# Optimization experiments

Measured on AMD Instinct MI355X. Metric: run time of the kernel, lower is better.

Reference implementation:

```python
import jax, jax.numpy as jnp
import numpy as np
import math

B, S, D, H, NL, DFF, C, K = 32, 1024, 512, 8, 6, 2048, 128, 8
HD = D // H  # head_dim = 64
EPS = 1e-5


def setup_inputs() -> dict:
    key = jax.random.key(0)
    ks = jax.random.split(key, 24)
    n = lambda k, shape, s=0.02: jax.random.normal(k, shape, jnp.float32) * s
    return {
        'theta': jax.random.uniform(ks[0], (B, S), jnp.float32, -math.pi, math.pi),
        'cond': jax.random.normal(ks[1], (B, C), jnp.float32),
        'attn_bias': jax.random.normal(ks[2], (H, S, S), jnp.float32) * 0.1,
        'embed_W': n(ks[3], (2, D)), 'embed_b': jnp.zeros((D,), jnp.float32),
        'ln1_g': jnp.ones((NL, D), jnp.float32), 'ln1_b': jnp.zeros((NL, D), jnp.float32),
        'ada1_W': n(ks[4], (NL, C, 2 * D)), 'ada1_b': jnp.zeros((NL, 2 * D), jnp.float32),
        'Wq': n(ks[5], (NL, D, D)), 'bq': jnp.zeros((NL, D), jnp.float32),
        'Wk': n(ks[6], (NL, D, D)), 'bk': jnp.zeros((NL, D), jnp.float32),
        'Wv': n(ks[7], (NL, D, D)), 'bv': jnp.zeros((NL, D), jnp.float32),
        'Wo': n(ks[8], (NL, D, D)), 'bo': jnp.zeros((NL, D), jnp.float32),
        'ln2_g': jnp.ones((NL, D), jnp.float32), 'ln2_b': jnp.zeros((NL, D), jnp.float32),
        'ada2_W': n(ks[9], (NL, C, 2 * D)), 'ada2_b': jnp.zeros((NL, 2 * D), jnp.float32),
        'W1': n(ks[10], (NL, D, DFF)), 'b1': jnp.zeros((NL, DFF), jnp.float32),
        'W2': n(ks[11], (NL, DFF, D)), 'b2': jnp.zeros((NL, D), jnp.float32),
        'fn_g': jnp.ones((D,), jnp.float32), 'fn_b': jnp.zeros((D,), jnp.float32),
        'head_W': n(ks[12], (D, 3 * K)), 'head_b': jnp.zeros((3 * K,), jnp.float32),
    }


def _layer_norm(x, g, b):
    m = jnp.mean(x, axis=-1, keepdims=True)
    v = jnp.mean(jnp.square(x - m), axis=-1, keepdims=True)
    return (x - m) * jax.lax.rsqrt(v + EPS) * g + b


def _adaln(x, cond, g, b, pW, pb):
    # AdaLN(x, c) = (1 + scale(c)) * LN(x) + shift(c)
    ss = cond @ pW + pb                      # [B, 2D]
    scale, shift = jnp.split(ss, 2, axis=-1)  # each [B, D]
    return (1.0 + scale[:, None, :]) * _layer_norm(x, g, b) + shift[:, None, :]


def reference(theta, cond, attn_bias, embed_W, embed_b, ln1_g, ln1_b, ada1_W, ada1_b,
              Wq, bq, Wk, bk, Wv, bv, Wo, bo, ln2_g, ln2_b, ada2_W, ada2_b,
              W1, b1, W2, b2, fn_g, fn_b, head_W, head_b):
    b_sz, s_len = theta.shape
    # circular embedding: (cos, sin) -> d_model
    emb_in = jnp.stack([jnp.cos(theta), jnp.sin(theta)], axis=-1)  # [B, S, 2]
    x = emb_in @ embed_W + embed_b                                 # [B, S, D]
    causal = jnp.triu(jnp.ones((s_len, s_len), bool), k=1)         # True above diag
    neg_inf = jnp.asarray(-jnp.inf, x.dtype)
    inv_sqrt = 1.0 / math.sqrt(HD)
    for i in range(NL):
        h = _adaln(x, cond, ln1_g[i], ln1_b[i], ada1_W[i], ada1_b[i])
        q = (h @ Wq[i] + bq[i]).reshape(b_sz, s_len, H, HD)
        k = (h @ Wk[i] + bk[i]).reshape(b_sz, s_len, H, HD)
        v = (h @ Wv[i] + bv[i]).reshape(b_sz, s_len, H, HD)
        scores = jnp.einsum('bqhd,bkhd->bhqk', q, k) * inv_sqrt  # [B, H, S, S]
        scores = scores + attn_bias[None]
        scores = jnp.where(causal[None, None], neg_inf, scores)
        attn = jax.nn.softmax(scores, axis=-1)
        ao = jnp.einsum('bhqk,bkhd->bqhd', attn, v).reshape(b_sz, s_len, D)
        x = x + (ao @ Wo[i] + bo[i])
        h2 = _adaln(x, cond, ln2_g[i], ln2_b[i], ada2_W[i], ada2_b[i])
        ff = jax.nn.gelu(h2 @ W1[i] + b1[i], approximate=False) @ W2[i] + b2[i]
        x = x + ff
    x = _layer_norm(x, fn_g, fn_b)
    return x @ head_W + head_b  # [B, S, 3K] mixture params (logw, mu, log-kappa)
```

## Files before the change

### kernel.cpp

```cpp
#include <hip/hip_runtime.h>


typedef short s8v __attribute__((ext_vector_type(8)));
typedef float f4v __attribute__((ext_vector_type(4)));
typedef unsigned u2v __attribute__((ext_vector_type(2)));
typedef unsigned u4v __attribute__((ext_vector_type(4)));

static __device__ __forceinline__ short f2bf(float f) {
  union { float f; unsigned u; } v; v.f = f;
  unsigned r = v.u + 0x7fffu + ((v.u >> 16) & 1u);
  return (short)(r >> 16);
}
static __device__ __forceinline__ float bf2f(unsigned short s) {
  union { unsigned u; float f; } v; v.u = ((unsigned)s) << 16;
  return v.f;
}
static __device__ __forceinline__ unsigned cvtpk(float lo, float hi) {
  unsigned r;
  asm("v_cvt_pk_bf16_f32 %0, %1, %2" : "=v"(r) : "v"(lo), "v"(hi));
  return r;
}
static __device__ __forceinline__ void gl_lds16(const short* g, short* l) {
  __builtin_amdgcn_global_load_lds(
      (const __attribute__((address_space(1))) unsigned int*)g,
      (__attribute__((address_space(3))) unsigned int*)l, 16, 0, 0);
}

__global__ void transpose_all_k(const float* __restrict__ Wq, const float* __restrict__ Wk,
                                const float* __restrict__ Wv, const float* __restrict__ Wo,
                                const float* __restrict__ W1, const float* __restrict__ W2,
                                int l, short* __restrict__ wbf) {
  int id = blockIdx.x;
  const float* in; short* out; int K, N, tx, ty;
  if (id < 1024) {
    int m = id >> 8, t = id & 255;
    in = (m == 0 ? Wq : m == 1 ? Wk : m == 2 ? Wv : Wo) + (size_t)l * 262144;
    out = wbf + (size_t)m * 262144;
    K = 512; N = 512; tx = t & 15; ty = t >> 4;
  } else if (id < 2048) {
    int t = id - 1024;
    in = W1 + (size_t)l * 1048576; out = wbf + 1048576;
    K = 512; N = 2048; tx = t & 63; ty = t >> 6;
  } else {
    int t = id - 2048;
    in = W2 + (size_t)l * 1048576; out = wbf + 2097152;
    K = 2048; N = 512; tx = t & 15; ty = t >> 4;
  }
  __shared__ float tb[32][33];
  int n0 = tx * 32, k0 = ty * 32;
  int cx = threadIdx.x & 31, cy = threadIdx.x >> 5;
#pragma unroll
  for (int r = 0; r < 4; r++)
    tb[cy + r * 8][cx] = in[(size_t)(k0 + cy + r * 8) * N + n0 + cx];
  __syncthreads();
#pragma unroll
  for (int r = 0; r < 4; r++)
    out[(size_t)(n0 + cy + r * 8) * K + k0 + cx] = f2bf(tb[cx][cy + r * 8]);
}

__global__ void bias_cvt_k(const float* __restrict__ in, short* __restrict__ out) {
  int i = blockIdx.x * 256 + threadIdx.x;
  float4 v = ((const float4*)in)[i];
  ushort4 o;
  o.x = (unsigned short)f2bf(v.x);
  o.y = (unsigned short)f2bf(v.y);
  o.z = (unsigned short)f2bf(v.z);
  o.w = (unsigned short)f2bf(v.w);
  ((ushort4*)out)[i] = o;
}

__global__ void hwt_k(const float* __restrict__ hW, short* __restrict__ hWT) {
  int i = blockIdx.x * 256 + threadIdx.x;
  int n = i >> 9, k = i & 511;
  hWT[i] = (n < 24) ? f2bf(hW[(size_t)k * 24 + n]) : (short)0;
}

__global__ void concat_qkvb_k(const float* bq, const float* bk, const float* bv, float* out) {
  int l = blockIdx.x;
  for (int i = threadIdx.x; i < 1536; i += 256) {
    float v = (i < 512) ? bq[l * 512 + i] * 0.125f
            : (i < 1024 ? bk[l * 512 + i - 512] : bv[l * 512 + i - 1024]);
    out[l * 1536 + i] = v;
  }
}

__global__ void cond_proj_k(const float* __restrict__ cond,
                            const float* __restrict__ a1W, const float* __restrict__ a1b,
                            const float* __restrict__ a2W, const float* __restrict__ a2b,
                            float* __restrict__ ss) {
  int lw = blockIdx.y, which = lw & 1, l = lw >> 1;
  const float* W = (which ? a2W : a1W) + (size_t)l * 128 * 1024;
  const float* bb = (which ? a2b : a1b) + (size_t)l * 1024;
  __shared__ float cs[32 * 128];
  for (int i = threadIdx.x; i < 32 * 128; i += 256) cs[i] = cond[i];
  __syncthreads();
  int n = blockIdx.x * 256 + threadIdx.x;
  float bias = bb[n];
  for (int g = 0; g < 4; g++) {
    float acc[8];
#pragma unroll
    for (int i = 0; i < 8; i++) acc[i] = 0.f;
    for (int c = 0; c < 128; c++) {
      float w = W[(size_t)c * 1024 + n];
#pragma unroll
      for (int i = 0; i < 8; i++) acc[i] += cs[(g * 8 + i) * 128 + c] * w;
    }
#pragma unroll
    for (int i = 0; i < 8; i++)
      ss[((size_t)lw * 32 + g * 8 + i) * 1024 + n] = acc[i] + bias;
  }
}

__global__ void embed_k(const float* __restrict__ theta, const float* __restrict__ eW,
                        const float* __restrict__ eb, float* __restrict__ x) {
  int row = blockIdx.x * 4 + (threadIdx.x >> 6), lane = threadIdx.x & 63;
  float th = theta[row], sn, cn;
  sincosf(th, &sn, &cn);
  int d = lane * 8;
  float* xo = x + (size_t)row * 512 + d;
#pragma unroll
  for (int i = 0; i < 8; i++) xo[i] = cn * eW[d + i] + sn * eW[512 + d + i] + eb[d + i];
}

template<bool HASDEL>
__global__ void adaln_k(float* __restrict__ x, const short* delta,
                        const float* __restrict__ ss,
                        const float* __restrict__ g, const float* __restrict__ be,
                        short* h) {
  int row = blockIdx.x * 4 + (threadIdx.x >> 6), lane = threadIdx.x & 63;
  int b = row >> 10;
  float* xr = x + (size_t)row * 512 + lane * 8;
  float4 va = ((const float4*)xr)[0], vb = ((const float4*)xr)[1];
  float v[8] = {va.x, va.y, va.z, va.w, vb.x, vb.y, vb.z, vb.w};
  if (HASDEL) {
    s8v dv = *(const s8v*)(delta + (size_t)row * 512 + lane * 8);
#pragma unroll
    for (int i = 0; i < 8; i++) v[i] += bf2f((unsigned short)dv[i]);
    float4 o0 = {v[0], v[1], v[2], v[3]}, o1 = {v[4], v[5], v[6], v[7]};
    ((float4*)xr)[0] = o0; ((float4*)xr)[1] = o1;
  }
  float sm = 0.f;
#pragma unroll
  for (int i = 0; i < 8; i++) sm += v[i];
#pragma unroll
  for (int off = 1; off < 64; off <<= 1) sm += __shfl_xor(sm, off);
  float mean = sm * (1.f / 512.f);
  float sq = 0.f;
#pragma unroll
  for (int i = 0; i < 8; i++) { float d = v[i] - mean; sq += d * d; }
#pragma unroll
  for (int off = 1; off < 64; off <<= 1) sq += __shfl_xor(sq, off);
  float rs = rsqrtf(sq * (1.f / 512.f) + 1e-5f);
  const float* sb = ss + (size_t)b * 1024 + lane * 8;
  const float* gp = g + lane * 8;
  const float* bp = be + lane * 8;
  s8v o;
#pragma unroll
  for (int i = 0; i < 8; i++) {
    float xh = (v[i] - mean) * rs * gp[i] + bp[i];
    o[i] = f2bf((1.f + sb[i]) * xh + sb[i + 512]);
  }
  *(s8v*)(h + (size_t)row * 512 + lane * 8) = o;
}

__global__ void fln_k(const float* __restrict__ x, const short* delta,
                      const float* __restrict__ g, const float* __restrict__ be,
                      short* h) {
  int row = blockIdx.x * 4 + (threadIdx.x >> 6), lane = threadIdx.x & 63;
  const float* xr = x + (size_t)row * 512 + lane * 8;
  float4 va = ((const float4*)xr)[0], vb = ((const float4*)xr)[1];
  float v[8] = {va.x, va.y, va.z, va.w, vb.x, vb.y, vb.z, vb.w};
  s8v dv = *(const s8v*)(delta + (size_t)row * 512 + lane * 8);
#pragma unroll
  for (int i = 0; i < 8; i++) v[i] += bf2f((unsigned short)dv[i]);
  float sm = 0.f;
#pragma unroll
  for (int i = 0; i < 8; i++) sm += v[i];
#pragma unroll
  for (int off = 1; off < 64; off <<= 1) sm += __shfl_xor(sm, off);
  float mean = sm * (1.f / 512.f);
  float sq = 0.f;
#pragma unroll
  for (int i = 0; i < 8; i++) { float d = v[i] - mean; sq += d * d; }
#pragma unroll
  for (int off = 1; off < 64; off <<= 1) sq += __shfl_xor(sq, off);
  float rs = rsqrtf(sq * (1.f / 512.f) + 1e-5f);
  const float* gp = g + lane * 8;
  const float* bp = be + lane * 8;
  s8v o;
#pragma unroll
  for (int i = 0; i < 8; i++) o[i] = f2bf((v[i] - mean) * rs * gp[i] + bp[i]);
  *(s8v*)(h + (size_t)row * 512 + lane * 8) = o;
}

template<int EPI>
__global__ __launch_bounds__(256) void gemm_bt_k(const short* __restrict__ A,
                                                 const short* __restrict__ BT,
                                                 const float* __restrict__ bias,
                                                 short* __restrict__ outb,
                                                 int N, int K) {
  __shared__ __align__(16) short lsA[2][128 * 32];
  __shared__ __align__(16) short lsB[2][128 * 32];
  int tid = threadIdx.x, lane = tid & 63, w = tid >> 6;
  int wm = w >> 1, wn = w & 1;
  int l15 = lane & 15, l4 = lane >> 4;
  int lrow = lane >> 2, lchunk = lane & 3;
  int nb = N >> 7;
  int bid = blockIdx.x;
  int xcd = bid & 7, rr = bid >> 3;
  int mloc = rr / nb, nidx = rr - mloc * nb;
  int m0 = (xcd * 32 + mloc) << 7, n0 = nidx << 7;
  f4v z4 = {0.f, 0.f, 0.f, 0.f};
  f4v acc[4][4];
#pragma unroll
  for (int i = 0; i < 4; i++)
#pragma unroll
    for (int j = 0; j < 4; j++) acc[i][j] = z4;

  auto STAGE = [&](int buf, int k0) {
#pragma unroll
    for (int t = 0; t < 2; t++) {
      int r0 = w * 32 + t * 16;
      int row = r0 + lrow;
      gl_lds16(A + (size_t)(m0 + row) * K + k0 + ((lchunk ^ (row & 3)) << 3), lsA[buf] + r0 * 32);
      gl_lds16(BT + (size_t)(n0 + row) * K + k0 + ((lchunk ^ (row & 3)) << 3), lsB[buf] + r0 * 32);
    }
  };

  int nk = K >> 5;
  STAGE(0, 0);
  for (int it = 0; it < nk; ++it) {
    int cur = it & 1;
    if (it + 1 < nk) {
      STAGE(cur ^ 1, (it + 1) << 5);
      asm volatile("s_waitcnt vmcnt(4)" ::: "memory");
    } else {
      asm volatile("s_waitcnt vmcnt(0)" ::: "memory");
    }
    __builtin_amdgcn_s_barrier();
    const short* lA = lsA[cur];
    const short* lB = lsB[cur];
    s8v af[4], bfr[4];
#pragma unroll
    for (int i = 0; i < 4; i++) {
      int ra = wm * 64 + i * 16 + l15;
      af[i] = *(const s8v*)(lA + ra * 32 + ((l4 ^ (ra & 3)) << 3));
      int rb = wn * 64 + i * 16 + l15;
      bfr[i] = *(const s8v*)(lB + rb * 32 + ((l4 ^ (rb & 3)) << 3));
    }
#pragma unroll
    for (int i = 0; i < 4; i++)
#pragma unroll
      for (int j = 0; j < 4; j++)
        acc[i][j] = __builtin_amdgcn_mfma_f32_16x16x32_bf16(af[i], bfr[j], acc[i][j], 0, 0, 0);
    __builtin_amdgcn_s_barrier();
  }
#pragma unroll
  for (int i = 0; i < 4; i++) {
    int gr0 = m0 + wm * 64 + i * 16 + l4 * 4;
#pragma unroll
    for (int j = 0; j < 4; j++) {
      int gc = n0 + wn * 64 + j * 16 + l15;
      float bv = bias[gc];
#pragma unroll
      for (int r = 0; r < 4; r++) {
        float v = acc[i][j][r] + bv;
        if (EPI == 1) {
          float t = v * (-1.5957691216f - 0.0713548162726f * v * v);
          v = v / (1.f + __expf(t));
        }
        outb[(size_t)(gr0 + r) * N + gc] = f2bf(v);
      }
    }
  }
}

__global__ __launch_bounds__(256) void qkvt_k(const short* __restrict__ A,
                                              const short* __restrict__ BT,
                                              const float* __restrict__ bias,
                                              short* __restrict__ qk,
                                              short* __restrict__ vtb) {
  __shared__ __align__(16) short lsA[2][128 * 32];
  __shared__ __align__(16) short lsB[2][128 * 32];
  int tid = threadIdx.x, lane = tid & 63, w = tid >> 6;
  int wm = w >> 1, wn = w & 1;
  int l15 = lane & 15, l4 = lane >> 4;
  int lrow = lane >> 2, lchunk = lane & 3;
  int bid = blockIdx.x;
  int xcd = bid & 7, rr = bid >> 3;
  int mloc = rr / 12, nidx = rr - mloc * 12;
  int m0 = (xcd * 32 + mloc) << 7, n0 = nidx << 7;
  bool isV = (n0 >= 1024);
  bool isQ = (n0 < 512);
  f4v z4 = {0.f, 0.f, 0.f, 0.f};
  f4v acc[4][4];
#pragma unroll
  for (int i = 0; i < 4; i++)
#pragma unroll
    for (int j = 0; j < 4; j++) acc[i][j] = z4;

  auto STAGE = [&](int buf, int k0) {
#pragma unroll
    for (int t = 0; t < 2; t++) {
      int r0 = w * 32 + t * 16;
      int row = r0 + lrow;
      gl_lds16(A + (size_t)(m0 + row) * 512 + k0 + ((lchunk ^ (row & 3)) << 3), lsA[buf] + r0 * 32);
      gl_lds16(BT + (size_t)(n0 + row) * 512 + k0 + ((lchunk ^ (row & 3)) << 3), lsB[buf] + r0 * 32);
    }
  };

  STAGE(0, 0);
  for (int it = 0; it < 16; ++it) {
    int cur = it & 1;
    if (it + 1 < 16) {
      STAGE(cur ^ 1, (it + 1) << 5);
      asm volatile("s_waitcnt vmcnt(4)" ::: "memory");
    } else {
      asm volatile("s_waitcnt vmcnt(0)" ::: "memory");
    }
    __builtin_amdgcn_s_barrier();
    const short* lA = lsA[cur];
    const short* lB = lsB[cur];
    s8v af[4], bfr[4];
#pragma unroll
    for (int i = 0; i < 4; i++) {
      int ra = wm * 64 + i * 16 + l15;
      af[i] = *(const s8v*)(lA + ra * 32 + ((l4 ^ (ra & 3)) << 3));
      int rb = wn * 64 + i * 16 + l15;
      bfr[i] = *(const s8v*)(lB + rb * 32 + ((l4 ^ (rb & 3)) << 3));
    }
    if (!isV) {
#pragma unroll
      for (int i = 0; i < 4; i++)
#pragma unroll
        for (int j = 0; j < 4; j++)
          acc[i][j] = __builtin_amdgcn_mfma_f32_16x16x32_bf16(af[i], bfr[j], acc[i][j], 0, 0, 0);
    } else {
#pragma unroll
      for (int j = 0; j < 4; j++)
#pragma unroll
        for (int i = 0; i < 4; i++)
          acc[j][i] = __builtin_amdgcn_mfma_f32_16x16x32_bf16(bfr[j], af[i], acc[j][i], 0, 0, 0);
    }
    __builtin_amdgcn_s_barrier();
  }
  if (!isV) {
    float scl = isQ ? 0.125f : 1.f;
#pragma unroll
    for (int i = 0; i < 4; i++) {
      int gr0 = m0 + wm * 64 + i * 16 + l4 * 4;
#pragma unroll
      for (int j = 0; j < 4; j++) {
        int gc = n0 + wn * 64 + j * 16 + l15;
        float bv = bias[gc];
#pragma unroll
        for (int r = 0; r < 4; r++)
          qk[(size_t)(gr0 + r) * 1024 + gc] = f2bf(acc[i][j][r] * scl + bv);
      }
    }
  } else {
    int b = m0 >> 10, s0 = m0 & 1023;
#pragma unroll
    for (int j = 0; j < 4; j++) {
      int col = n0 + wn * 64 + j * 16 + l4 * 4;
#pragma unroll
      for (int i = 0; i < 4; i++) {
        int scol = s0 + wm * 64 + i * 16 + l15;
#pragma unroll
        for (int r = 0; r < 4; r++) {
          float v = acc[j][i][r] + bias[col + r];
          vtb[((size_t)b * 512 + col - 1024 + r) * 1024 + scol] = f2bf(v);
        }
      }
    }
  }
}

__global__ __launch_bounds__(256, 4) void attn_k(const short* __restrict__ qk,
                                                 const short* __restrict__ vt,
                                                 const short* __restrict__ biasNT,
                                                 short* __restrict__ ao) {
  __shared__ __align__(16) short Kl[2][64 * 64];
  __shared__ __align__(16) short Vl[2][64 * 64];
  int tid = threadIdx.x, lane = tid & 63, w = tid >> 6;
  int bid = blockIdx.x;
  int qt = 7 - (bid >> 8), b = (bid >> 3) & 31, h = bid & 7;
  int l15 = lane & 15, l4 = lane >> 4;
  int lrow = lane >> 3, lchunk = lane & 7;

  f4v z4 = {0.f, 0.f, 0.f, 0.f};
  s8v qf[2][2];
#pragma unroll
  for (int g = 0; g < 2; g++) {
    const short* qp = qk + (size_t)(b * 1024 + qt * 128 + g * 64 + w * 16 + l15) * 1024 + h * 64;
    qf[g][0] = *(const s8v*)(qp + l4 * 8);
    qf[g][1] = *(const s8v*)(qp + 32 + l4 * 8);
  }
  f4v o[2][4], lac[2];
#pragma unroll
  for (int g = 0; g < 2; g++) {
    lac[g] = z4;
#pragma unroll
    for (int j = 0; j < 4; j++) o[g][j] = z4;
  }
  s8v ones;
#pragma unroll
  for (int e = 0; e < 8; e++) ones[e] = (short)0x3F80;

  auto STAGE = [&](int buf, int kt) {
#pragma unroll
    for (int t = 0; t < 2; t++) {
      int r0 = (w * 2 + t) * 8;
      int row = r0 + lrow;
      gl_lds16(qk + (size_t)(b * 1024 + kt * 64 + row) * 1024 + 512 + h * 64 +
                   ((lchunk ^ (row & 7)) << 3),
               &Kl[buf][r0 * 64]);
      gl_lds16(vt + (size_t)(b * 512 + h * 64 + row) * 1024 + kt * 64 +
                   ((lchunk ^ (row & 7)) << 3),
               &Vl[buf][r0 * 64]);
    }
  };

  int nkt = 2 * qt + 2;
  STAGE(0, 0);
  for (int kt = 0; kt < nkt; kt++) {
    int cur = kt & 1;
    ushort4 bh[2][4];
#pragma unroll
    for (int g = 0; g < 2; g++) {
      if (kt > 2 * qt + g) continue;
      const short* bp = biasNT + ((size_t)h * 1024 + qt * 128 + g * 64 + w * 16 + l15) * 1024 +
                        kt * 64 + l4 * 4;
#pragma unroll
      for (int j = 0; j < 4; j++) bh[g][j] = *(const ushort4*)(bp + j * 16);
    }
    __builtin_amdgcn_sched_barrier(0);
    if (kt + 1 < nkt) {
      STAGE(cur ^ 1, kt + 1);
      asm volatile("s_waitcnt vmcnt(4)" ::: "memory");
    } else {
      asm volatile("s_waitcnt vmcnt(0)" ::: "memory");
    }
    __builtin_amdgcn_s_barrier();
    const short* Kc = &Kl[cur][0];
    const short* Vc = &Vl[cur][0];
#pragma unroll
    for (int g = 0; g < 2; g++) {
      int diag = 2 * qt + g;
      if (kt > diag) continue;
      f4v s[4];
#pragma unroll
      for (int j = 0; j < 4; j++) {
        f4v bc;
        bc[0] = bf2f(bh[g][j].x); bc[1] = bf2f(bh[g][j].y);
        bc[2] = bf2f(bh[g][j].z); bc[3] = bf2f(bh[g][j].w);
        int kr = j * 16 + l15;
        s8v kf0 = *(const s8v*)(Kc + kr * 64 + ((l4 ^ (kr & 7)) << 3));
        s8v kf1 = *(const s8v*)(Kc + kr * 64 + (((l4 + 4) ^ (kr & 7)) << 3));
        s[j] = __builtin_amdgcn_mfma_f32_16x16x32_bf16(kf0, qf[g][0], bc, 0, 0, 0);
        s[j] = __builtin_amdgcn_mfma_f32_16x16x32_bf16(kf1, qf[g][1], s[j], 0, 0, 0);
      }
      if (kt == diag) {
#pragma unroll
        for (int j = 0; j < 4; j++)
#pragma unroll
          for (int r = 0; r < 4; r++) {
            int kk = j * 16 + l4 * 4 + r, qq = w * 16 + l15;
            s[j][r] = (kk > qq) ? 0.f : __expf(s[j][r]);
          }
      } else {
#pragma unroll
        for (int j = 0; j < 4; j++)
#pragma unroll
          for (int r = 0; r < 4; r++) s[j][r] = __expf(s[j][r]);
      }
      unsigned X0[4], X1[4];
#pragma unroll
      for (int j = 0; j < 4; j++) {
        X0[j] = cvtpk(s[j][0], s[j][1]);
        X1[j] = cvtpk(s[j][2], s[j][3]);
      }
      u2v a0 = __builtin_amdgcn_permlane32_swap(X0[0], X0[1], false, false);
      u2v a1 = __builtin_amdgcn_permlane16_swap(a0[0], a0[1], false, false);
      u2v b0 = __builtin_amdgcn_permlane32_swap(X1[0], X1[1], false, false);
      u2v b1 = __builtin_amdgcn_permlane16_swap(b0[0], b0[1], false, false);
      u2v c0 = __builtin_amdgcn_permlane32_swap(X0[2], X0[3], false, false);
      u2v c1 = __builtin_amdgcn_permlane16_swap(c0[0], c0[1], false, false);
      u2v d0 = __builtin_amdgcn_permlane32_swap(X1[2], X1[3], false, false);
      u2v d1 = __builtin_amdgcn_permlane16_swap(d0[0], d0[1], false, false);
      u4v P0 = {a1[0], b1[0], a1[1], b1[1]};
      u4v P1 = {c1[0], d1[0], c1[1], d1[1]};
      s8v pf0 = __builtin_bit_cast(s8v, P0);
      s8v pf1 = __builtin_bit_cast(s8v, P1);
      lac[g] = __builtin_amdgcn_mfma_f32_16x16x32_bf16(pf0, ones, lac[g], 0, 0, 0);
      lac[g] = __builtin_amdgcn_mfma_f32_16x16x32_bf16(pf1, ones, lac[g], 0, 0, 0);
#pragma unroll
      for (int j = 0; j < 4; j++) {
        int dr = j * 16 + l15;
        s8v vf0 = *(const s8v*)(Vc + dr * 64 + ((l4 ^ (dr & 7)) << 3));
        s8v vf1 = *(const s8v*)(Vc + dr * 64 + (((l4 + 4) ^ (dr & 7)) << 3));
        o[g][j] = __builtin_amdgcn_mfma_f32_16x16x32_bf16(pf0, vf0, o[g][j], 0, 0, 0);
        o[g][j] = __builtin_amdgcn_mfma_f32_16x16x32_bf16(pf1, vf1, o[g][j], 0, 0, 0);
      }
    }
    __builtin_amdgcn_s_barrier();
  }
#pragma unroll
  for (int g = 0; g < 2; g++)
#pragma unroll
    for (int r = 0; r < 4; r++) {
      float rl = 1.f / lac[g][r];
      int qr = qt * 128 + g * 64 + w * 16 + l4 * 4 + r;
#pragma unroll
      for (int j = 0; j < 4; j++) {
        int d = j * 16 + l15;
        ao[(size_t)(b * 1024 + qr) * 512 + h * 64 + d] = f2bf(o[g][j][r] * rl);
      }
    }
}

__global__ __launch_bounds__(256) void head_k(const short* __restrict__ X,
                                              const short* __restrict__ hWT,
                                              const float* __restrict__ hb,
                                              float* __restrict__ out) {
  __shared__ __align__(16) short lA[128 * 64];
  int tid = threadIdx.x, lane = tid & 63, w = tid >> 6;
  int l15 = lane & 15, l4 = lane >> 4;
  int lrow = lane >> 3, lchunk = lane & 7;
  int m0 = blockIdx.x * 128;
  f4v z4 = {0.f, 0.f, 0.f, 0.f};
  f4v acc[2][2];
#pragma unroll
  for (int i = 0; i < 2; i++)
#pragma unroll
    for (int j = 0; j < 2; j++) acc[i][j] = z4;

  for (int k0 = 0; k0 < 512; k0 += 64) {
#pragma unroll
    for (int t = 0; t < 4; t++) {
      int r0 = (w * 4 + t) * 8;
      int row = r0 + lrow;
      gl_lds16(X + (size_t)(m0 + row) * 512 + k0 + ((lchunk ^ (row & 7)) << 3), lA + r0 * 64);
    }
    __syncthreads();
#pragma unroll
    for (int kk = 0; kk < 2; kk++) {
      s8v af[2], bfr[2];
#pragma unroll
      for (int i = 0; i < 2; i++) {
        int ra = w * 32 + i * 16 + l15;
        af[i] = *(const s8v*)(lA + ra * 64 + (((l4 + kk * 4) ^ (ra & 7)) << 3));
      }
#pragma unroll
      for (int j = 0; j < 2; j++)
        bfr[j] = *(const s8v*)(hWT + (size_t)(j * 16 + l15) * 512 + k0 + kk * 32 + l4 * 8);
#pragma unroll
      for (int i = 0; i < 2; i++)
#pragma unroll
        for (int j = 0; j < 2; j++)
          acc[i][j] = __builtin_amdgcn_mfma_f32_16x16x32_bf16(af[i], bfr[j], acc[i][j], 0, 0, 0);
    }
    __syncthreads();
  }
#pragma unroll
  for (int i = 0; i < 2; i++) {
#pragma unroll
    for (int j = 0; j < 2; j++) {
      int col = j * 16 + l15;
      if (col < 24) {
        float bv = hb[col];
#pragma unroll
        for (int r = 0; r < 4; r++) {
          int row = m0 + w * 32 + i * 16 + l4 * 4 + r;
          out[(size_t)row * 24 + col] = acc[i][j][r] + bv;
        }
      }
    }
  }
}

extern "C" void kernel_launch(void* const* d_in, const int* in_sizes, int n_in,
                              void* d_out, int out_size, void* d_ws, size_t ws_size,
                              hipStream_t stream) {
  (void)in_sizes; (void)n_in; (void)out_size;
  const float* theta   = (const float*)d_in[0];
  const float* cond    = (const float*)d_in[1];
  const float* attn_b  = (const float*)d_in[2];
  const float* embed_W = (const float*)d_in[3];
  const float* embed_b = (const float*)d_in[4];
  const float* ln1_g   = (const float*)d_in[5];
  const float* ln1_b   = (const float*)d_in[6];
  const float* ada1_W  = (const float*)d_in[7];
  const float* ada1_b  = (const float*)d_in[8];
  const float* Wq      = (const float*)d_in[9];
  const float* bq      = (const float*)d_in[10];
  const float* Wk      = (const float*)d_in[11];
  const float* bk      = (const float*)d_in[12];
  const float* Wv      = (const float*)d_in[13];
  const float* bv      = (const float*)d_in[14];
  const float* Wo      = (const float*)d_in[15];
  const float* bo      = (const float*)d_in[16];
  const float* ln2_g   = (const float*)d_in[17];
  const float* ln2_b   = (const float*)d_in[18];
  const float* ada2_W  = (const float*)d_in[19];
  const float* ada2_b  = (const float*)d_in[20];
  const float* W1      = (const float*)d_in[21];
  const float* b1      = (const float*)d_in[22];
  const float* W2      = (const float*)d_in[23];
  const float* b2      = (const float*)d_in[24];
  const float* fn_g    = (const float*)d_in[25];
  const float* fn_b    = (const float*)d_in[26];
  const float* head_W  = (const float*)d_in[27];
  const float* head_b  = (const float*)d_in[28];

  const size_t REQ = 242814976ull;
  const size_t REQ2 = 259592192ull;
  if (ws_size < REQ) return;
  bool bias_once = (ws_size >= REQ2);

  char* ws = (char*)d_ws;
  float* xw    = (float*)(ws + 0ull);
  short* qk    = (short*)(ws + 67108864ull);
  short* vtb   = (short*)(ws + 134217728ull);
  short* biasT = (short*)(ws + (bias_once ? 242814976ull : 167772160ull));
  short* qf    = (short*)(ws + 67108864ull);
  short* hbuf  = (short*)(ws + 201326592ull);
  short* wbf   = (short*)(ws + 234881024ull);
  float* ssb   = (float*)(ws + 241172480ull);
  float* bqkv  = (float*)(ws + 242745344ull);
  short* hWT   = (short*)(ws + 242782208ull);

  concat_qkvb_k<<<6, 256, 0, stream>>>(bq, bk, bv, bqkv);
  cond_proj_k<<<dim3(4, 12), 256, 0, stream>>>(cond, ada1_W, ada1_b, ada2_W, ada2_b, ssb);
  hwt_k<<<64, 256, 0, stream>>>(head_W, hWT);
  embed_k<<<8192, 256, 0, stream>>>(theta, embed_W, embed_b, xw);
  if (bias_once) bias_cvt_k<<<8192, 256, 0, stream>>>(attn_b, biasT);

  for (int l = 0; l < 6; l++) {
    transpose_all_k<<<3072, 256, 0, stream>>>(Wq, Wk, Wv, Wo, W1, W2, l, wbf);
    if (!bias_once) bias_cvt_k<<<8192, 256, 0, stream>>>(attn_b, biasT);

    if (l == 0)
      adaln_k<false><<<8192, 256, 0, stream>>>(xw, nullptr, ssb + (size_t)(l * 2) * 32768,
                                               ln1_g + l * 512, ln1_b + l * 512, hbuf);
    else
      adaln_k<true><<<8192, 256, 0, stream>>>(xw, hbuf, ssb + (size_t)(l * 2) * 32768,
                                              ln1_g + l * 512, ln1_b + l * 512, hbuf);
    qkvt_k<<<3072, 256, 0, stream>>>(hbuf, wbf, bqkv + l * 1536, qk, vtb);
    attn_k<<<2048, 256, 0, stream>>>(qk, vtb, biasT, hbuf);
    gemm_bt_k<0><<<1024, 256, 0, stream>>>(hbuf, wbf + 786432, bo + l * 512, vtb, 512, 512);
    adaln_k<true><<<8192, 256, 0, stream>>>(xw, vtb, ssb + (size_t)(l * 2 + 1) * 32768,
                                            ln2_g + l * 512, ln2_b + l * 512, hbuf);
    gemm_bt_k<1><<<4096, 256, 0, stream>>>(hbuf, wbf + 1048576, b1 + l * 2048, qf, 2048, 512);
    gemm_bt_k<0><<<1024, 256, 0, stream>>>(qf, wbf + 2097152, b2 + l * 512, hbuf, 512, 2048);
  }
  fln_k<<<8192, 256, 0, stream>>>(xw, hbuf, fn_g, fn_b, hbuf);
  head_k<<<256, 256, 0, stream>>>(hbuf, hWT, head_b, (float*)d_out);
}
```

Baseline: 2.861 ms.

## Use 256x256-tile GEMMs with 8 waves and a 4-stage LDS pipeline

Replaces the 128x128 four-wave GEMM and QKV kernels with 256x256 tiles on 512-thread blocks. Each wave computes a 128x64 sub-tile, and operands are staged through a 4-deep ring of LDS buffers, with A and B loads interleaved between two half-MFMA phases and MFMA sections run at raised wave priority. The LDS layout changes to a fragment-ordered layout with no XOR swizzle. This is meant to raise arithmetic intensity and hide global latency better, at the cost of 128 KB of LDS per block, fewer blocks (256 for the N=512 GEMMs), and higher register pressure.

```diff
diff --git a/kernel.cpp b/kernel.cpp
--- a/kernel.cpp
+++ b/kernel.cpp
@@ -194,70 +194,91 @@
 }
 
 template<int EPI>
-__global__ __launch_bounds__(256) void gemm_bt_k(const short* __restrict__ A,
-                                                 const short* __restrict__ BT,
-                                                 const float* __restrict__ bias,
-                                                 short* __restrict__ outb,
-                                                 int N, int K) {
-  __shared__ __align__(16) short lsA[2][128 * 32];
-  __shared__ __align__(16) short lsB[2][128 * 32];
+__global__ __launch_bounds__(512, 2) void gemm256_k(const short* __restrict__ A,
+                                                    const short* __restrict__ BT,
+                                                    const float* __restrict__ bias,
+                                                    short* __restrict__ outb,
+                                                    int N, int K) {
+  __shared__ __align__(16) short lsA[4][8192];
+  __shared__ __align__(16) short lsB[4][8192];
   int tid = threadIdx.x, lane = tid & 63, w = tid >> 6;
-  int wm = w >> 1, wn = w & 1;
+  int wm = w >> 2, wn = w & 3;
   int l15 = lane & 15, l4 = lane >> 4;
-  int lrow = lane >> 2, lchunk = lane & 3;
-  int nb = N >> 7;
+  int nn = N >> 8;
   int bid = blockIdx.x;
   int xcd = bid & 7, rr = bid >> 3;
-  int mloc = rr / nb, nidx = rr - mloc * nb;
-  int m0 = (xcd * 32 + mloc) << 7, n0 = nidx << 7;
+  int mloc = rr / nn, nidx = rr - mloc * nn;
+  int m0 = (xcd * 16 + mloc) << 8, n0 = nidx << 8;
+
+  const short* sA0 = A + (size_t)(m0 + w * 32 + l15) * K + l4 * 8;
+  const short* sA1 = sA0 + (size_t)16 * K;
+  const short* sB0 = BT + (size_t)(n0 + w * 32 + l15) * K + l4 * 8;
+  const short* sB1 = sB0 + (size_t)16 * K;
+
   f4v z4 = {0.f, 0.f, 0.f, 0.f};
-  f4v acc[4][4];
-#pragma unroll
-  for (int i = 0; i < 4; i++)
+  f4v acc[8][4];
+#pragma unroll
+  for (int i = 0; i < 8; i++)
 #pragma unroll
     for (int j = 0; j < 4; j++) acc[i][j] = z4;
 
-  auto STAGE = [&](int buf, int k0) {
-#pragma unroll
-    for (int t = 0; t < 2; t++) {
-      int r0 = w * 32 + t * 16;
-      int row = r0 + lrow;
-      gl_lds16(A + (size_t)(m0 + row) * K + k0 + ((lchunk ^ (row & 3)) << 3), lsA[buf] + r0 * 32);
-      gl_lds16(BT + (size_t)(n0 + row) * K + k0 + ((lchunk ^ (row & 3)) << 3), lsB[buf] + r0 * 32);
-    }
+  auto STA = [&](int t) {
+    short* d = lsA[t & 3] + w * 1024;
+    int ko = t * 32;
+    gl_lds16(sA0 + ko, d); gl_lds16(sA1 + ko, d + 512);
   };
-
-  int nk = K >> 5;
-  STAGE(0, 0);
-  for (int it = 0; it < nk; ++it) {
-    int cur = it & 1;
-    if (it + 1 < nk) {
-      STAGE(cur ^ 1, (it + 1) << 5);
-      asm volatile("s_waitcnt vmcnt(4)" ::: "memory");
-    } else {
-      asm volatile("s_waitcnt vmcnt(0)" ::: "memory");
-    }
-    __builtin_amdgcn_s_barrier();
-    const short* lA = lsA[cur];
-    const short* lB = lsB[cur];
-    s8v af[4], bfr[4];
-#pragma unroll
-    for (int i = 0; i < 4; i++) {
-      int ra = wm * 64 + i * 16 + l15;
-      af[i] = *(const s8v*)(lA + ra * 32 + ((l4 ^ (ra & 3)) << 3));
-      int rb = wn * 64 + i * 16 + l15;
-      bfr[i] = *(const s8v*)(lB + rb * 32 + ((l4 ^ (rb & 3)) << 3));
-    }
+  auto STB = [&](int t) {
+    short* d = lsB[t & 3] + w * 1024;
+    int ko = t * 32;
+    gl_lds16(sB0 + ko, d); gl_lds16(sB1 + ko, d + 512);
+  };
+
+  int NT = K >> 5;
+  STA(0); STB(0); STA(1); STB(1); STA(2); STB(2);
+  asm volatile("s_waitcnt vmcnt(8)" ::: "memory");
+  __builtin_amdgcn_s_barrier();
+
+  for (int t = 0; t < NT; ++t) {
+    const short* At = lsA[t & 3] + (wm * 8) * 512 + lane * 8;
+    const short* Bt = lsB[t & 3] + (wn * 4) * 512 + lane * 8;
+    s8v bfrag[4], afrag[4];
+#pragma unroll
+    for (int j = 0; j < 4; j++) bfrag[j] = *(const s8v*)(Bt + j * 512);
+#pragma unroll
+    for (int i = 0; i < 4; i++) afrag[i] = *(const s8v*)(At + i * 512);
+    if (t + 3 < NT) STA(t + 3);
+    __builtin_amdgcn_s_barrier();
+    asm volatile("s_waitcnt lgkmcnt(0)" ::: "memory");
+    __builtin_amdgcn_sched_barrier(0);
+    __builtin_amdgcn_s_setprio(1);
 #pragma unroll
     for (int i = 0; i < 4; i++)
 #pragma unroll
       for (int j = 0; j < 4; j++)
-        acc[i][j] = __builtin_amdgcn_mfma_f32_16x16x32_bf16(af[i], bfr[j], acc[i][j], 0, 0, 0);
-    __builtin_amdgcn_s_barrier();
-  }
-#pragma unroll
-  for (int i = 0; i < 4; i++) {
-    int gr0 = m0 + wm * 64 + i * 16 + l4 * 4;
+        acc[i][j] = __builtin_amdgcn_mfma_f32_16x16x32_bf16(afrag[i], bfrag[j], acc[i][j], 0, 0, 0);
+    __builtin_amdgcn_s_setprio(0);
+    __builtin_amdgcn_s_barrier();
+#pragma unroll
+    for (int i = 0; i < 4; i++) afrag[i] = *(const s8v*)(At + (4 + i) * 512);
+    if (t + 3 < NT) STB(t + 3);
+    __builtin_amdgcn_s_barrier();
+    asm volatile("s_waitcnt lgkmcnt(0)" ::: "memory");
+    __builtin_amdgcn_sched_barrier(0);
+    __builtin_amdgcn_s_setprio(1);
+#pragma unroll
+    for (int i = 0; i < 4; i++)
+#pragma unroll
+      for (int j = 0; j < 4; j++)
+        acc[4 + i][j] = __builtin_amdgcn_mfma_f32_16x16x32_bf16(afrag[i], bfrag[j], acc[4 + i][j], 0, 0, 0);
+    __builtin_amdgcn_s_setprio(0);
+    if (t + 4 <= NT) { asm volatile("s_waitcnt vmcnt(8)" ::: "memory"); }
+    else if (t + 3 == NT) { asm volatile("s_waitcnt vmcnt(4)" ::: "memory"); }
+    else if (t + 2 == NT) { asm volatile("s_waitcnt vmcnt(0)" ::: "memory"); }
+    __builtin_amdgcn_s_barrier();
+  }
+#pragma unroll
+  for (int i = 0; i < 8; i++) {
+    int gr0 = m0 + wm * 128 + i * 16 + l4 * 4;
 #pragma unroll
     for (int j = 0; j < 4; j++) {
       int gc = n0 + wn * 64 + j * 16 + l15;
@@ -266,8 +287,8 @@
       for (int r = 0; r < 4; r++) {
         float v = acc[i][j][r] + bv;
         if (EPI == 1) {
-          float t = v * (-1.5957691216f - 0.0713548162726f * v * v);
-          v = v / (1.f + __expf(t));
+          float tg = v * (-1.5957691216f - 0.0713548162726f * v * v);
+          v = v / (1.f + __expf(tg));
         }
         outb[(size_t)(gr0 + r) * N + gc] = f2bf(v);
       }
@@ -275,80 +296,110 @@
   }
 }
 
-__global__ __launch_bounds__(256) void qkvt_k(const short* __restrict__ A,
-                                              const short* __restrict__ BT,
-                                              const float* __restrict__ bias,
-                                              short* __restrict__ qk,
-                                              short* __restrict__ vtb) {
-  __shared__ __align__(16) short lsA[2][128 * 32];
-  __shared__ __align__(16) short lsB[2][128 * 32];
+__global__ __launch_bounds__(512, 2) void qkvt256_k(const short* __restrict__ A,
+                                                    const short* __restrict__ BT,
+                                                    const float* __restrict__ bias,
+                                                    short* __restrict__ qk,
+                                                    short* __restrict__ vtb) {
+  __shared__ __align__(16) short lsA[4][8192];
+  __shared__ __align__(16) short lsB[4][8192];
   int tid = threadIdx.x, lane = tid & 63, w = tid >> 6;
-  int wm = w >> 1, wn = w & 1;
+  int wm = w >> 2, wn = w & 3;
   int l15 = lane & 15, l4 = lane >> 4;
-  int lrow = lane >> 2, lchunk = lane & 3;
   int bid = blockIdx.x;
   int xcd = bid & 7, rr = bid >> 3;
-  int mloc = rr / 12, nidx = rr - mloc * 12;
-  int m0 = (xcd * 32 + mloc) << 7, n0 = nidx << 7;
+  int mloc = rr / 6, nidx = rr - mloc * 6;
+  int m0 = (xcd * 16 + mloc) << 8, n0 = nidx << 8;
   bool isV = (n0 >= 1024);
   bool isQ = (n0 < 512);
+
+  const short* sA0 = A + (size_t)(m0 + w * 32 + l15) * 512 + l4 * 8;
+  const short* sA1 = sA0 + (size_t)16 * 512;
+  const short* sB0 = BT + (size_t)(n0 + w * 32 + l15) * 512 + l4 * 8;
+  const short* sB1 = sB0 + (size_t)16 * 512;
+
   f4v z4 = {0.f, 0.f, 0.f, 0.f};
-  f4v acc[4][4];
-#pragma unroll
-  for (int i = 0; i < 4; i++)
+  f4v acc[8][4];
+#pragma unroll
+  for (int i = 0; i < 8; i++)
 #pragma unroll
     for (int j = 0; j < 4; j++) acc[i][j] = z4;
 
-  auto STAGE = [&](int buf, int k0) {
-#pragma unroll
-    for (int t = 0; t < 2; t++) {
-      int r0 = w * 32 + t * 16;
-      int row = r0 + lrow;
-      gl_lds16(A + (size_t)(m0 + row) * 512 + k0 + ((lchunk ^ (row & 3)) << 3), lsA[buf] + r0 * 32);
-      gl_lds16(BT + (size_t)(n0 + row) * 512 + k0 + ((lchunk ^ (row & 3)) << 3), lsB[buf] + r0 * 32);
-    }
+  auto STA = [&](int t) {
+    short* d = lsA[t & 3] + w * 1024;
+    int ko = t * 32;
+    gl_lds16(sA0 + ko, d); gl_lds16(sA1 + ko, d + 512);
   };
-
-  STAGE(0, 0);
-  for (int it = 0; it < 16; ++it) {
-    int cur = it & 1;
-    if (it + 1 < 16) {
-      STAGE(cur ^ 1, (it + 1) << 5);
-      asm volatile("s_waitcnt vmcnt(4)" ::: "memory");
+  auto STB = [&](int t) {
+    short* d = lsB[t & 3] + w * 1024;
+    int ko = t * 32;
+    gl_lds16(sB0 + ko, d); gl_lds16(sB1 + ko, d + 512);
+  };
+
+  const int NT = 16;
+  STA(0); STB(0); STA(1); STB(1); STA(2); STB(2);
+  asm volatile("s_waitcnt vmcnt(8)" ::: "memory");
+  __builtin_amdgcn_s_barrier();
+
+  for (int t = 0; t < NT; ++t) {
+    const short* At = lsA[t & 3] + (wm * 8) * 512 + lane * 8;
+    const short* Bt = lsB[t & 3] + (wn * 4) * 512 + lane * 8;
+    s8v bfrag[4], afrag[4];
+#pragma unroll
+    for (int j = 0; j < 4; j++) bfrag[j] = *(const s8v*)(Bt + j * 512);
+#pragma unroll
+    for (int i = 0; i < 4; i++) afrag[i] = *(const s8v*)(At + i * 512);
+    if (t + 3 < NT) STA(t + 3);
+    __builtin_amdgcn_s_barrier();
+    asm volatile("s_waitcnt lgkmcnt(0)" ::: "memory");
+    __builtin_amdgcn_sched_barrier(0);
+    __builtin_amdgcn_s_setprio(1);
+    if (!isV) {
+#pragma unroll
+      for (int i = 0; i < 4; i++)
+#pragma unroll
+        for (int j = 0; j < 4; j++)
+          acc[i][j] = __builtin_amdgcn_mfma_f32_16x16x32_bf16(afrag[i], bfrag[j], acc[i][j], 0, 0, 0);
     } else {
-      asm volatile("s_waitcnt vmcnt(0)" ::: "memory");
-    }
-    __builtin_amdgcn_s_barrier();
-    const short* lA = lsA[cur];
-    const short* lB = lsB[cur];
-    s8v af[4], bfr[4];
-#pragma unroll
-    for (int i = 0; i < 4; i++) {
-      int ra = wm * 64 + i * 16 + l15;
-      af[i] = *(const s8v*)(lA + ra * 32 + ((l4 ^ (ra & 3)) << 3));
-      int rb = wn * 64 + i * 16 + l15;
-      bfr[i] = *(const s8v*)(lB + rb * 32 + ((l4 ^ (rb & 3)) << 3));
-    }
+#pragma unroll
+      for (int j = 0; j < 4; j++)
+#pragma unroll
+        for (int i = 0; i < 4; i++)
+          acc[i][j] = __builtin_amdgcn_mfma_f32_16x16x32_bf16(bfrag[j], afrag[i], acc[i][j], 0, 0, 0);
+    }
+    __builtin_amdgcn_s_setprio(0);
+    __builtin_amdgcn_s_barrier();
+#pragma unroll
+    for (int i = 0; i < 4; i++) afrag[i] = *(const s8v*)(At + (4 + i) * 512);
+    if (t + 3 < NT) STB(t + 3);
+    __builtin_amdgcn_s_barrier();
+    asm volatile("s_waitcnt lgkmcnt(0)" ::: "memory");
+    __builtin_amdgcn_sched_barrier(0);
+    __builtin_amdgcn_s_setprio(1);
     if (!isV) {
 #pragma unroll
       for (int i = 0; i < 4; i++)
 #pragma unroll
         for (int j = 0; j < 4; j++)
-          acc[i][j] = __builtin_amdgcn_mfma_f32_16x16x32_bf16(af[i], bfr[j], acc[i][j], 0, 0, 0);
+          acc[4 + i][j] = __builtin_amdgcn_mfma_f32_16x16x32_bf16(afrag[i], bfrag[j], acc[4 + i][j], 0, 0, 0);
     } else {
 #pragma unroll
       for (int j = 0; j < 4; j++)
 #pragma unroll
         for (int i = 0; i < 4; i++)
-          acc[j][i] = __builtin_amdgcn_mfma_f32_16x16x32_bf16(bfr[j], af[i], acc[j][i], 0, 0, 0);
-    }
+          acc[4 + i][j] = __builtin_amdgcn_mfma_f32_16x16x32_bf16(bfrag[j], afrag[i], acc[4 + i][j], 0, 0, 0);
+    }
+    __builtin_amdgcn_s_setprio(0);
+    if (t + 4 <= NT) { asm volatile("s_waitcnt vmcnt(8)" ::: "memory"); }
+    else if (t + 3 == NT) { asm volatile("s_waitcnt vmcnt(4)" ::: "memory"); }
+    else if (t + 2 == NT) { asm volatile("s_waitcnt vmcnt(0)" ::: "memory"); }
     __builtin_amdgcn_s_barrier();
   }
   if (!isV) {
     float scl = isQ ? 0.125f : 1.f;
 #pragma unroll
-    for (int i = 0; i < 4; i++) {
-      int gr0 = m0 + wm * 64 + i * 16 + l4 * 4;
+    for (int i = 0; i < 8; i++) {
+      int gr0 = m0 + wm * 128 + i * 16 + l4 * 4;
 #pragma unroll
       for (int j = 0; j < 4; j++) {
         int gc = n0 + wn * 64 + j * 16 + l15;
@@ -361,15 +412,15 @@
   } else {
     int b = m0 >> 10, s0 = m0 & 1023;
 #pragma unroll
-    for (int j = 0; j < 4; j++) {
-      int col = n0 + wn * 64 + j * 16 + l4 * 4;
-#pragma unroll
-      for (int i = 0; i < 4; i++) {
-        int scol = s0 + wm * 64 + i * 16 + l15;
+    for (int i = 0; i < 8; i++) {
+      int scol = s0 + wm * 128 + i * 16 + l15;
+#pragma unroll
+      for (int j = 0; j < 4; j++) {
+        int nb = n0 + wn * 64 + j * 16 + l4 * 4;
 #pragma unroll
         for (int r = 0; r < 4; r++) {
-          float v = acc[j][i][r] + bias[col + r];
-          vtb[((size_t)b * 512 + col - 1024 + r) * 1024 + scol] = f2bf(v);
+          float v = acc[i][j][r] + bias[nb + r];
+          vtb[((size_t)b * 512 + (nb - 1024) + r) * 1024 + scol] = f2bf(v);
         }
       }
     }
@@ -646,13 +697,13 @@
     else
       adaln_k<true><<<8192, 256, 0, stream>>>(xw, hbuf, ssb + (size_t)(l * 2) * 32768,
                                               ln1_g + l * 512, ln1_b + l * 512, hbuf);
-    qkvt_k<<<3072, 256, 0, stream>>>(hbuf, wbf, bqkv + l * 1536, qk, vtb);
+    qkvt256_k<<<768, 512, 0, stream>>>(hbuf, wbf, bqkv + l * 1536, qk, vtb);
     attn_k<<<2048, 256, 0, stream>>>(qk, vtb, biasT, hbuf);
-    gemm_bt_k<0><<<1024, 256, 0, stream>>>(hbuf, wbf + 786432, bo + l * 512, vtb, 512, 512);
+    gemm256_k<0><<<256, 512, 0, stream>>>(hbuf, wbf + 786432, bo + l * 512, vtb, 512, 512);
     adaln_k<true><<<8192, 256, 0, stream>>>(xw, vtb, ssb + (size_t)(l * 2 + 1) * 32768,
                                             ln2_g + l * 512, ln2_b + l * 512, hbuf);
-    gemm_bt_k<1><<<4096, 256, 0, stream>>>(hbuf, wbf + 1048576, b1 + l * 2048, qf, 2048, 512);
-    gemm_bt_k<0><<<1024, 256, 0, stream>>>(qf, wbf + 2097152, b2 + l * 512, hbuf, 512, 2048);
+    gemm256_k<1><<<1024, 512, 0, stream>>>(hbuf, wbf + 1048576, b1 + l * 2048, qf, 2048, 512);
+    gemm256_k<0><<<256, 512, 0, stream>>>(qf, wbf + 2097152, b2 + l * 512, hbuf, 512, 2048);
   }
   fln_k<<<8192, 256, 0, stream>>>(xw, hbuf, fn_g, fn_b, hbuf);
   head_k<<<256, 256, 0, stream>>>(hbuf, hWT, head_b, (float*)d_out);
```

Result: no change. 2.894 ms (+1.2%).

## Triple-buffer GEMM LDS staging with fragment-ordered layout and MFMA priority

Applied to the files above, without the earlier changes.

Both the generic GEMM and the fused QKV GEMM move from double to triple buffering of the LDS tiles, keeping two k-tiles of global-to-LDS loads in flight. The staging layout changes so each lane's 16-byte load lands where an MFMA fragment read expects it, which removes the XOR-swizzle address math on both the load and read sides. An explicit lgkmcnt wait, a sched_barrier and s_setprio around the MFMA block are added to favour matrix work. LDS use rises by half, which may lower occupancy, and the new layout may shift bank-conflict behaviour.

```diff
diff --git a/kernel.cpp b/kernel.cpp
--- a/kernel.cpp
+++ b/kernel.cpp
@@ -199,17 +199,22 @@
                                                  const float* __restrict__ bias,
                                                  short* __restrict__ outb,
                                                  int N, int K) {
-  __shared__ __align__(16) short lsA[2][128 * 32];
-  __shared__ __align__(16) short lsB[2][128 * 32];
+  __shared__ __align__(16) short lsA[3][4096];
+  __shared__ __align__(16) short lsB[3][4096];
   int tid = threadIdx.x, lane = tid & 63, w = tid >> 6;
   int wm = w >> 1, wn = w & 1;
   int l15 = lane & 15, l4 = lane >> 4;
-  int lrow = lane >> 2, lchunk = lane & 3;
   int nb = N >> 7;
   int bid = blockIdx.x;
   int xcd = bid & 7, rr = bid >> 3;
   int mloc = rr / nb, nidx = rr - mloc * nb;
   int m0 = (xcd * 32 + mloc) << 7, n0 = nidx << 7;
+
+  const short* sA0 = A + (size_t)(m0 + w * 32 + l15) * K + l4 * 8;
+  const short* sA1 = sA0 + (size_t)16 * K;
+  const short* sB0 = BT + (size_t)(n0 + w * 32 + l15) * K + l4 * 8;
+  const short* sB1 = sB0 + (size_t)16 * K;
+
   f4v z4 = {0.f, 0.f, 0.f, 0.f};
   f4v acc[4][4];
 #pragma unroll
@@ -217,42 +222,48 @@
 #pragma unroll
     for (int j = 0; j < 4; j++) acc[i][j] = z4;
 
-  auto STAGE = [&](int buf, int k0) {
-#pragma unroll
-    for (int t = 0; t < 2; t++) {
-      int r0 = w * 32 + t * 16;
-      int row = r0 + lrow;
-      gl_lds16(A + (size_t)(m0 + row) * K + k0 + ((lchunk ^ (row & 3)) << 3), lsA[buf] + r0 * 32);
-      gl_lds16(BT + (size_t)(n0 + row) * K + k0 + ((lchunk ^ (row & 3)) << 3), lsB[buf] + r0 * 32);
-    }
+  auto STAGE = [&](int t) {
+    int slot = t % 3;
+    int ko = t << 5;
+    short* dA = lsA[slot] + w * 1024;
+    short* dB = lsB[slot] + w * 1024;
+    gl_lds16(sA0 + ko, dA); gl_lds16(sA1 + ko, dA + 512);
+    gl_lds16(sB0 + ko, dB); gl_lds16(sB1 + ko, dB + 512);
   };
 
-  int nk = K >> 5;
-  STAGE(0, 0);
-  for (int it = 0; it < nk; ++it) {
-    int cur = it & 1;
-    if (it + 1 < nk) {
-      STAGE(cur ^ 1, (it + 1) << 5);
+  int NT = K >> 5;
+  STAGE(0); STAGE(1);
+  asm volatile("s_waitcnt vmcnt(4)" ::: "memory");
+  __builtin_amdgcn_s_barrier();
+
+  for (int t = 0; t < NT; ++t) {
+    if (t + 2 < NT) {
+      STAGE(t + 2);
+      asm volatile("s_waitcnt vmcnt(8)" ::: "memory");
+    } else if (t + 1 < NT) {
       asm volatile("s_waitcnt vmcnt(4)" ::: "memory");
     } else {
       asm volatile("s_waitcnt vmcnt(0)" ::: "memory");
     }
     __builtin_amdgcn_s_barrier();
-    const short* lA = lsA[cur];
-    const short* lB = lsB[cur];
+    int slot = t % 3;
+    const short* At = lsA[slot] + (wm * 4) * 512 + lane * 8;
+    const short* Bt = lsB[slot] + (wn * 4) * 512 + lane * 8;
     s8v af[4], bfr[4];
 #pragma unroll
     for (int i = 0; i < 4; i++) {
-      int ra = wm * 64 + i * 16 + l15;
-      af[i] = *(const s8v*)(lA + ra * 32 + ((l4 ^ (ra & 3)) << 3));
-      int rb = wn * 64 + i * 16 + l15;
-      bfr[i] = *(const s8v*)(lB + rb * 32 + ((l4 ^ (rb & 3)) << 3));
-    }
+      af[i] = *(const s8v*)(At + i * 512);
+      bfr[i] = *(const s8v*)(Bt + i * 512);
+    }
+    asm volatile("s_waitcnt lgkmcnt(0)" ::: "memory");
+    __builtin_amdgcn_sched_barrier(0);
+    __builtin_amdgcn_s_setprio(1);
 #pragma unroll
     for (int i = 0; i < 4; i++)
 #pragma unroll
       for (int j = 0; j < 4; j++)
         acc[i][j] = __builtin_amdgcn_mfma_f32_16x16x32_bf16(af[i], bfr[j], acc[i][j], 0, 0, 0);
+    __builtin_amdgcn_s_setprio(0);
     __builtin_amdgcn_s_barrier();
   }
 #pragma unroll
@@ -266,8 +277,8 @@
       for (int r = 0; r < 4; r++) {
         float v = acc[i][j][r] + bv;
         if (EPI == 1) {
-          float t = v * (-1.5957691216f - 0.0713548162726f * v * v);
-          v = v / (1.f + __expf(t));
+          float tg = v * (-1.5957691216f - 0.0713548162726f * v * v);
+          v = v / (1.f + __expf(tg));
         }
         outb[(size_t)(gr0 + r) * N + gc] = f2bf(v);
       }
@@ -280,18 +291,23 @@
                                               const float* __restrict__ bias,
                                               short* __restrict__ qk,
                                               short* __restrict__ vtb) {
-  __shared__ __align__(16) short lsA[2][128 * 32];
-  __shared__ __align__(16) short lsB[2][128 * 32];
+  __shared__ __align__(16) short lsA[3][4096];
+  __shared__ __align__(16) short lsB[3][4096];
   int tid = threadIdx.x, lane = tid & 63, w = tid >> 6;
   int wm = w >> 1, wn = w & 1;
   int l15 = lane & 15, l4 = lane >> 4;
-  int lrow = lane >> 2, lchunk = lane & 3;
   int bid = blockIdx.x;
   int xcd = bid & 7, rr = bid >> 3;
   int mloc = rr / 12, nidx = rr - mloc * 12;
   int m0 = (xcd * 32 + mloc) << 7, n0 = nidx << 7;
   bool isV = (n0 >= 1024);
   bool isQ = (n0 < 512);
+
+  const short* sA0 = A + (size_t)(m0 + w * 32 + l15) * 512 + l4 * 8;
+  const short* sA1 = sA0 + (size_t)16 * 512;
+  const short* sB0 = BT + (size_t)(n0 + w * 32 + l15) * 512 + l4 * 8;
+  const short* sB1 = sB0 + (size_t)16 * 512;
+
   f4v z4 = {0.f, 0.f, 0.f, 0.f};
   f4v acc[4][4];
 #pragma unroll
@@ -299,36 +315,42 @@
 #pragma unroll
     for (int j = 0; j < 4; j++) acc[i][j] = z4;
 
-  auto STAGE = [&](int buf, int k0) {
-#pragma unroll
-    for (int t = 0; t < 2; t++) {
-      int r0 = w * 32 + t * 16;
-      int row = r0 + lrow;
-      gl_lds16(A + (size_t)(m0 + row) * 512 + k0 + ((lchunk ^ (row & 3)) << 3), lsA[buf] + r0 * 32);
-      gl_lds16(BT + (size_t)(n0 + row) * 512 + k0 + ((lchunk ^ (row & 3)) << 3), lsB[buf] + r0 * 32);
-    }
+  auto STAGE = [&](int t) {
+    int slot = t % 3;
+    int ko = t << 5;
+    short* dA = lsA[slot] + w * 1024;
+    short* dB = lsB[slot] + w * 1024;
+    gl_lds16(sA0 + ko, dA); gl_lds16(sA1 + ko, dA + 512);
+    gl_lds16(sB0 + ko, dB); gl_lds16(sB1 + ko, dB + 512);
   };
 
-  STAGE(0, 0);
-  for (int it = 0; it < 16; ++it) {
-    int cur = it & 1;
-    if (it + 1 < 16) {
-      STAGE(cur ^ 1, (it + 1) << 5);
+  const int NT = 16;
+  STAGE(0); STAGE(1);
+  asm volatile("s_waitcnt vmcnt(4)" ::: "memory");
+  __builtin_amdgcn_s_barrier();
+
+  for (int t = 0; t < NT; ++t) {
+    if (t + 2 < NT) {
+      STAGE(t + 2);
+      asm volatile("s_waitcnt vmcnt(8)" ::: "memory");
+    } else if (t + 1 < NT) {
       asm volatile("s_waitcnt vmcnt(4)" ::: "memory");
     } else {
       asm volatile("s_waitcnt vmcnt(0)" ::: "memory");
     }
     __builtin_amdgcn_s_barrier();
-    const short* lA = lsA[cur];
-    const short* lB = lsB[cur];
+    int slot = t % 3;
+    const short* At = lsA[slot] + (wm * 4) * 512 + lane * 8;
+    const short* Bt = lsB[slot] + (wn * 4) * 512 + lane * 8;
     s8v af[4], bfr[4];
 #pragma unroll
     for (int i = 0; i < 4; i++) {
-      int ra = wm * 64 + i * 16 + l15;
-      af[i] = *(const s8v*)(lA + ra * 32 + ((l4 ^ (ra & 3)) << 3));
-      int rb = wn * 64 + i * 16 + l15;
-      bfr[i] = *(const s8v*)(lB + rb * 32 + ((l4 ^ (rb & 3)) << 3));
-    }
+      af[i] = *(const s8v*)(At + i * 512);
+      bfr[i] = *(const s8v*)(Bt + i * 512);
+    }
+    asm volatile("s_waitcnt lgkmcnt(0)" ::: "memory");
+    __builtin_amdgcn_sched_barrier(0);
+    __builtin_amdgcn_s_setprio(1);
     if (!isV) {
 #pragma unroll
       for (int i = 0; i < 4; i++)
@@ -342,6 +364,7 @@
         for (int i = 0; i < 4; i++)
           acc[j][i] = __builtin_amdgcn_mfma_f32_16x16x32_bf16(bfr[j], af[i], acc[j][i], 0, 0, 0);
     }
+    __builtin_amdgcn_s_setprio(0);
     __builtin_amdgcn_s_barrier();
   }
   if (!isV) {
```

Result: slower. 3.742 ms (+30.8%).
